# Kernel optimization log

Measured on AMD Instinct MI355X. Metric: run time of the kernel, lower is better.

## Reference

```python
import jax, jax.numpy as jnp
import numpy as np

D_HEAD = 64
KV_HEADS = 8
Q_HEADS = 32
ROPE_BASE = 10000.0


def rope(x):
    # x: (B, S, H, D); pairs are interleaved along last dim, matching torch view(...,D//2,2)
    B, S, H, D = x.shape
    inv_freq = 1.0 / (ROPE_BASE ** (jnp.arange(0, D, 2, dtype=jnp.float32) / D))
    theta = jnp.arange(S, dtype=jnp.float32)[:, None] * inv_freq[None, :]  # (S, D/2)
    cos = jnp.cos(theta)[None, :, None, :]
    sin = jnp.sin(theta)[None, :, None, :]
    xf = x.astype(jnp.float32).reshape(B, S, H, D // 2, 2)
    x1, x2 = xf[..., 0], xf[..., 1]
    out = jnp.stack((x1 * cos - x2 * sin, x1 * sin + x2 * cos), axis=-1)
    return out.reshape(B, S, H, D).astype(x.dtype)


def setup_inputs() -> dict:
    key = jax.random.key(0)
    ks = jax.random.split(key, 5)
    B, S, D = 2, 2048, 2048
    scale = 1.0 / np.sqrt(D)
    return {
        "x": jax.random.normal(ks[0], (B, S, D), dtype=jnp.float32),
        "Wq": jax.random.normal(ks[1], (Q_HEADS * D_HEAD, D), dtype=jnp.float32) * scale,
        "Wk": jax.random.normal(ks[2], (KV_HEADS * D_HEAD, D), dtype=jnp.float32) * scale,
        "Wv": jax.random.normal(ks[3], (KV_HEADS * D_HEAD, D), dtype=jnp.float32) * scale,
        "Wo": jax.random.normal(ks[4], (D, D), dtype=jnp.float32) * scale,
    }


def reference(x, Wq, Wk, Wv, Wo):
    B, S, D = x.shape
    G = Q_HEADS // KV_HEADS  # query heads per kv head

    Q = (x @ Wq.T).reshape(B, S, Q_HEADS, D_HEAD)
    K = (x @ Wk.T).reshape(B, S, KV_HEADS, D_HEAD)
    V = (x @ Wv.T).reshape(B, S, KV_HEADS, D_HEAD)

    Q = rope(Q)
    K = rope(K)

    # (B, KV, G, S, Dh): group g of kv head h corresponds to q head h*G+g,
    # exactly matching repeat_interleave of K/V along head dim.
    Q = Q.transpose(0, 2, 1, 3).reshape(B, KV_HEADS, G, S, D_HEAD)
    K = K.transpose(0, 2, 1, 3)  # (B, KV, S, Dh)
    V = V.transpose(0, 2, 1, 3)

    scores = jnp.einsum("bkgsd,bktd->bkgst", Q, K) / np.sqrt(D_HEAD).astype(np.float32)
    causal_mask = jnp.tril(jnp.ones((S, S), dtype=bool))
    scores = jnp.where(causal_mask, scores, -jnp.inf)
    probs = jax.nn.softmax(scores, axis=-1)
    attn = jnp.einsum("bkgst,bktd->bkgsd", probs, V)

    attn = attn.reshape(B, Q_HEADS, S, D_HEAD).transpose(0, 2, 1, 3).reshape(B, S, D)
    return attn @ Wo.T
```

## Files before the change

### kernel.cpp

```cpp
#include <hip/hip_runtime.h>
#include <stdint.h>

#define S_LEN   2048
#define D_MODEL 2048
#define DKV     512

typedef __attribute__((ext_vector_type(8))) short short8;
typedef __attribute__((ext_vector_type(4))) float f32x4;

__device__ static inline unsigned short f2bf(float f) {
  unsigned u = __builtin_bit_cast(unsigned, f);
  u += 0x7FFFu + ((u >> 16) & 1u);
  return (unsigned short)(u >> 16);
}
__device__ static inline float bf2f(unsigned short h) {
  return __builtin_bit_cast(float, ((unsigned)h) << 16);
}
__device__ static inline unsigned packtrunc2(float f0, float f1) {
  return __builtin_amdgcn_perm(__builtin_bit_cast(unsigned, f1),
                               __builtin_bit_cast(unsigned, f0), 0x07060302u);
}

__device__ static inline void gload_lds16(const void* g, void* lds) {
  __builtin_amdgcn_global_load_lds((const __attribute__((address_space(1))) void*)g,
                                   (__attribute__((address_space(3))) void*)lds,
                                   16, 0, 0);
}

__global__ __launch_bounds__(256) void cvt_all_kernel(
    const float* __restrict__ x, const float* __restrict__ wq, const float* __restrict__ wk,
    const float* __restrict__ wv, const float* __restrict__ wo,
    unsigned short* __restrict__ xb, unsigned short* __restrict__ wqb,
    unsigned short* __restrict__ wkb, unsigned short* __restrict__ wvb,
    unsigned short* __restrict__ wob) {
  int i = blockIdx.x * 256 + threadIdx.x;
  const float* s; unsigned short* d;
  if (i < 1048576)      { s = x;  d = xb;  }
  else if (i < 1572864) { s = wq; d = wqb; i -= 1048576; }
  else if (i < 1703936) { s = wk; d = wkb; i -= 1572864; }
  else if (i < 1835008) { s = wv; d = wvb; i -= 1703936; }
  else                  { s = wo; d = wob; i -= 1835008; }
  const float4 a = ((const float4*)s)[i * 2];
  const float4 b = ((const float4*)s)[i * 2 + 1];
  unsigned short u[8] = {f2bf(a.x), f2bf(a.y), f2bf(a.z), f2bf(a.w),
                         f2bf(b.x), f2bf(b.y), f2bf(b.z), f2bf(b.w)};
  *(uint4*)(d + (size_t)i * 8) = *(const uint4*)u;
}

__device__ static inline void storeC(unsigned short* C, size_t idx, float v) { C[idx] = f2bf(v); }
__device__ static inline void storeC(float* C, size_t idx, float v) { C[idx] = v; }

template <int CMODE, typename CT>
__device__ __forceinline__ void gemm128_body(const unsigned short* A, int lda,
                                             const unsigned short* B, int ldb,
                                             CT* C, int ldc,
                                             int m0, int n0, int Kdim,
                                             unsigned short* As, unsigned short* Bs) {
  const int tid  = threadIdx.x;
  const int lane = tid & 63;
  const int w    = tid >> 6;
  const int wm   = w >> 1, wn = w & 1;
  const int lcol = lane & 15;
  const int lq   = lane >> 4;

  f32x4 acc[4][4] = {};

  for (int k0 = 0; k0 < Kdim; k0 += 32) {
    __syncthreads();
#pragma unroll
    for (int i = 0; i < 2; ++i) {
      const int c  = i * 4 + w;
      const int e  = c * 512 + lane * 8;
      const int rr = e >> 5;
      const int cc = e & 31;
      gload_lds16(A + (size_t)(m0 + rr) * lda + (k0 + cc), As + c * 512);
      gload_lds16(B + (size_t)(n0 + rr) * ldb + (k0 + cc), Bs + c * 512);
    }
    __syncthreads();

    short8 af[4], bfr[4];
#pragma unroll
    for (int mi = 0; mi < 4; ++mi)
      af[mi] = *(const short8*)&As[(wm * 64 + mi * 16 + lcol) * 32 + lq * 8];
#pragma unroll
    for (int ni = 0; ni < 4; ++ni)
      bfr[ni] = *(const short8*)&Bs[(wn * 64 + ni * 16 + lcol) * 32 + lq * 8];
#pragma unroll
    for (int mi = 0; mi < 4; ++mi)
#pragma unroll
      for (int ni = 0; ni < 4; ++ni)
        acc[mi][ni] = __builtin_amdgcn_mfma_f32_16x16x32_bf16(af[mi], bfr[ni], acc[mi][ni], 0, 0, 0);
  }
#pragma unroll
  for (int mi = 0; mi < 4; ++mi)
#pragma unroll
    for (int ni = 0; ni < 4; ++ni)
#pragma unroll
      for (int r = 0; r < 4; ++r) {
        const int row = m0 + wm * 64 + mi * 16 + lq * 4 + r;
        const int col = n0 + wn * 64 + ni * 16 + lcol;
        if constexpr (CMODE == 1) {
          C[((size_t)((row >> 11) * 512 + col)) * 2048 + (row & 2047)] = f2bf(acc[mi][ni][r]);
        } else {
          storeC(C, (size_t)row * ldc + col, acc[mi][ni][r]);
        }
      }
}

__global__ __launch_bounds__(256) void qkv_gemm_kernel(
    const unsigned short* __restrict__ x,
    const unsigned short* __restrict__ Wq, const unsigned short* __restrict__ Wk,
    const unsigned short* __restrict__ Wv,
    unsigned short* __restrict__ Qo, unsigned short* __restrict__ Ko, unsigned short* __restrict__ Vt) {
  __shared__ unsigned short As[128 * 32];
  __shared__ unsigned short Bs[128 * 32];
  const int tn = blockIdx.x;
  const int m0 = blockIdx.y * 128;
  if (tn < 16) {
    gemm128_body<0>(x, D_MODEL, Wq, D_MODEL, Qo, D_MODEL, m0, tn * 128, D_MODEL, As, Bs);
  } else if (tn < 20) {
    gemm128_body<0>(x, D_MODEL, Wk, D_MODEL, Ko, DKV, m0, (tn - 16) * 128, D_MODEL, As, Bs);
  } else {
    gemm128_body<1>(x, D_MODEL, Wv, D_MODEL, Vt, DKV, m0, (tn - 20) * 128, D_MODEL, As, Bs);
  }
}

__global__ __launch_bounds__(256) void oproj_gemm_kernel(
    const unsigned short* __restrict__ A, const unsigned short* __restrict__ Wo,
    float* __restrict__ C) {
  __shared__ unsigned short As[128 * 32];
  __shared__ unsigned short Bs[128 * 32];
  gemm128_body<0>(A, D_MODEL, Wo, D_MODEL, C, D_MODEL,
                  blockIdx.y * 128, blockIdx.x * 128, D_MODEL, As, Bs);
}

__global__ __launch_bounds__(256) void rope_both_kernel(unsigned short* __restrict__ Qb,
                                                        unsigned short* __restrict__ Kb) {
  int idx = blockIdx.x * 256 + threadIdx.x;
  unsigned short* X; int lgHalf; float scale;
  if (idx < 4194304) { X = Qb; lgHalf = 10; scale = 0.1803368801111244f; }
  else               { X = Kb; lgHalf = 8;  scale = 1.0f; idx -= 4194304; }
  const int half = 1 << lgHalf;
  const int r  = idx >> lgHalf;
  const int cp = idx & (half - 1);
  const int i  = cp & 31;
  const int s  = r & (S_LEN - 1);
  const float inv = exp2f(-13.287712379549449f * (float)(2 * i) * (1.0f / 64.0f));
  const float th  = (float)s * inv;
  const float c = cosf(th), sn = sinf(th);
  unsigned short* p = X + ((size_t)r << (lgHalf + 1)) + 2 * cp;
  const float x0 = bf2f(p[0]), x1 = bf2f(p[1]);
  p[0] = f2bf((x0 * c - x1 * sn) * scale);
  p[1] = f2bf((x0 * sn + x1 * c) * scale);
}

__global__ __launch_bounds__(256, 2) void attn_kernel(const unsigned short* __restrict__ Q,
                                                      const unsigned short* __restrict__ K,
                                                      const unsigned short* __restrict__ Vt,
                                                      unsigned short* __restrict__ O) {
  const int hq = blockIdx.y;
  const int bb = blockIdx.z;
  const int hk = hq >> 2;
  const int tid  = threadIdx.x;
  const int lane = tid & 63;
  const int w    = tid >> 6;
  const int lcol = lane & 15;
  const int lq   = lane >> 4;
  const int trow = tid >> 2;
  const int tq   = (tid & 3) * 16;

  const int X = blockIdx.x;
  const int qt[4] = {X, 15 - X, 16 + X, 31 - X};

  __shared__ unsigned short Ks[64 * 72];
  __shared__ unsigned short Vts[64 * 72];
  __shared__ unsigned short Ps[4][64 * 72];

  const int prow = w * 16 + lcol;

  uint4 kp0, kp1, vp0, vp1;
  {
    const unsigned short* gk = K + ((size_t)(bb * S_LEN + trow)) * DKV + hk * 64 + tq;
    kp0 = *(const uint4*)gk; kp1 = *(const uint4*)(gk + 8);
    const unsigned short* gv = Vt + ((size_t)(bb * DKV + hk * 64 + trow)) * S_LEN + tq;
    vp0 = *(const uint4*)gv; vp1 = *(const uint4*)(gv + 8);
  }

#pragma unroll
  for (int j = 0; j < 4; ++j) {
    const unsigned short* g = Q + ((size_t)(bb * S_LEN + qt[j] * 64 + trow)) * D_MODEL + hq * 64 + tq;
    *(uint4*)&Ps[j][trow * 72 + tq]     = *(const uint4*)g;
    *(uint4*)&Ps[j][trow * 72 + tq + 8] = *(const uint4*)(g + 8);
  }
  asm volatile("s_waitcnt lgkmcnt(0)" ::: "memory");

  short8 qf[4][2];
#pragma unroll
  for (int j = 0; j < 4; ++j)
#pragma unroll
    for (int ks = 0; ks < 2; ++ks)
      qf[j][ks] = *(const short8*)&Ps[j][prow * 72 + ks * 32 + lq * 8];

  f32x4 Oacc[4][4] = {};
  float lacc[4] = {0.f, 0.f, 0.f, 0.f};

  const int tmax = qt[3];
  for (int t = 0; t <= tmax; ++t) {
    __syncthreads();
    *(uint4*)&Ks[trow * 72 + tq]      = kp0;
    *(uint4*)&Ks[trow * 72 + tq + 8]  = kp1;
    *(uint4*)&Vts[trow * 72 + tq]     = vp0;
    *(uint4*)&Vts[trow * 72 + tq + 8] = vp1;
    if (t < tmax) {
      const int t1 = (t + 1) * 64;
      const unsigned short* gk = K + ((size_t)(bb * S_LEN + t1 + trow)) * DKV + hk * 64 + tq;
      kp0 = *(const uint4*)gk; kp1 = *(const uint4*)(gk + 8);
      const unsigned short* gv = Vt + ((size_t)(bb * DKV + hk * 64 + trow)) * S_LEN + t1 + tq;
      vp0 = *(const uint4*)gv; vp1 = *(const uint4*)(gv + 8);
    }
    __syncthreads();

    bool act[4];
#pragma unroll
    for (int j = 0; j < 4; ++j) act[j] = (t <= qt[j]);

    f32x4 S[4][4] = {};
#pragma unroll
    for (int ks = 0; ks < 2; ++ks)
#pragma unroll
      for (int nt = 0; nt < 4; ++nt) {
        const short8 kf = *(const short8*)&Ks[(nt * 16 + lcol) * 72 + ks * 32 + lq * 8];
#pragma unroll
        for (int j = 0; j < 4; ++j)
          if (act[j])
            S[j][nt] = __builtin_amdgcn_mfma_f32_16x16x32_bf16(kf, qf[j][ks], S[j][nt], 0, 0, 0);
      }

#pragma unroll
    for (int j = 0; j < 4; ++j) {
      if (!act[j]) continue;
      if (t == qt[j]) {
        const int qrow = qt[j] * 64 + prow;
#pragma unroll
        for (int nt = 0; nt < 4; ++nt)
#pragma unroll
          for (int r = 0; r < 4; ++r) {
            const int key = t * 64 + nt * 16 + lq * 4 + r;
            if (key > qrow) S[j][nt][r] = -1e30f;
          }
      }
#pragma unroll
      for (int nt = 0; nt < 4; ++nt) {
        const float p0 = __builtin_amdgcn_exp2f(S[j][nt][0]);
        const float p1 = __builtin_amdgcn_exp2f(S[j][nt][1]);
        const float p2 = __builtin_amdgcn_exp2f(S[j][nt][2]);
        const float p3 = __builtin_amdgcn_exp2f(S[j][nt][3]);
        lacc[j] += (p0 + p1) + (p2 + p3);
        unsigned u2[2] = {packtrunc2(p0, p1), packtrunc2(p2, p3)};
        *(uint2*)&Ps[j][prow * 72 + nt * 16 + lq * 4] = *(const uint2*)u2;
      }
    }
    asm volatile("s_waitcnt lgkmcnt(0)" ::: "memory");

#pragma unroll
    for (int ks = 0; ks < 2; ++ks) {
      short8 pf[4];
#pragma unroll
      for (int j = 0; j < 4; ++j)
        if (act[j]) pf[j] = *(const short8*)&Ps[j][prow * 72 + ks * 32 + lq * 8];
#pragma unroll
      for (int dt = 0; dt < 4; ++dt) {
        const short8 vf = *(const short8*)&Vts[(dt * 16 + lcol) * 72 + ks * 32 + lq * 8];
#pragma unroll
        for (int j = 0; j < 4; ++j)
          if (act[j])
            Oacc[j][dt] = __builtin_amdgcn_mfma_f32_16x16x32_bf16(vf, pf[j], Oacc[j][dt], 0, 0, 0);
      }
    }
  }

#pragma unroll
  for (int j = 0; j < 4; ++j) {
    float l = lacc[j];
    l += __shfl_xor(l, 16);
    l += __shfl_xor(l, 32);
    const float inv = 1.0f / l;
    const int qrow = qt[j] * 64 + prow;
#pragma unroll
    for (int dt = 0; dt < 4; ++dt) {
      unsigned short u[4] = {f2bf(Oacc[j][dt][0] * inv), f2bf(Oacc[j][dt][1] * inv),
                             f2bf(Oacc[j][dt][2] * inv), f2bf(Oacc[j][dt][3] * inv)};
      *(uint2*)&O[(size_t)(bb * S_LEN + qrow) * D_MODEL + hq * 64 + dt * 16 + lq * 4] =
          *(const uint2*)u;
    }
  }
}

extern "C" void kernel_launch(void* const* d_in, const int* in_sizes, int n_in,
                              void* d_out, int out_size, void* d_ws, size_t ws_size,
                              hipStream_t stream) {
  const float* x  = (const float*)d_in[0];
  const float* Wq = (const float*)d_in[1];
  const float* Wk = (const float*)d_in[2];
  const float* Wv = (const float*)d_in[3];
  const float* Wo = (const float*)d_in[4];
  float* out = (float*)d_out;

  unsigned short* Qb  = (unsigned short*)d_ws;
  unsigned short* Kb  = Qb  + (size_t)4096 * 2048;
  unsigned short* Vtg = Kb  + (size_t)4096 * 512;
  unsigned short* Ab  = Vtg + (size_t)1024 * 2048;
  unsigned short* xb  = Ab  + (size_t)4096 * 2048;
  unsigned short* Wqb = xb  + (size_t)4096 * 2048;
  unsigned short* Wkb = Wqb + (size_t)2048 * 2048;
  unsigned short* Wvb = Wkb + (size_t)512 * 2048;
  unsigned short* Wob = Wvb + (size_t)512 * 2048;

  cvt_all_kernel<<<9216, 256, 0, stream>>>(x, Wq, Wk, Wv, Wo, xb, Wqb, Wkb, Wvb, Wob);

  qkv_gemm_kernel<<<dim3(24, 32), 256, 0, stream>>>(xb, Wqb, Wkb, Wvb, Qb, Kb, Vtg);
  rope_both_kernel<<<20480, 256, 0, stream>>>(Qb, Kb);
  attn_kernel<<<dim3(8, 32, 2), 256, 0, stream>>>(Qb, Kb, Vtg, Ab);
  oproj_gemm_kernel<<<dim3(16, 32), 256, 0, stream>>>(Ab, Wob, out);
}
```

Before: 307.9 us.

## Rewrite QKV and output-projection GEMMs with larger tiles and a 4-stage LDS pipeline

Replaces the 128x128 single-buffered GEMM with 256x256 (QKV) and 128x256 (output projection) tiles run by 512-thread blocks. Global-to-LDS loads are issued three tiles ahead into a 4-buffer ring, paced by explicit vmcnt waits and raw barriers, and the LDS layout is XOR-swizzled to avoid bank conflicts. Block IDs are remapped for L2 locality and MFMA sections are wrapped in raised wave priority. This is meant to hide memory latency and raise data reuse, at the cost of a large dynamic LDS footprint (128KB/96KB), hardcoded K=2048 loop counts and fewer blocks in the grid.

```diff
diff --git a/kernel.cpp b/kernel.cpp
--- a/kernel.cpp
+++ b/kernel.cpp
@@ -25,6 +25,15 @@
   __builtin_amdgcn_global_load_lds((const __attribute__((address_space(1))) void*)g,
                                    (__attribute__((address_space(3))) void*)lds,
                                    16, 0, 0);
+}
+
+template <int N>
+__device__ __forceinline__ void wait_vm() {
+  if constexpr (N == 8)      asm volatile("s_waitcnt vmcnt(8)" ::: "memory");
+  else if constexpr (N == 6) asm volatile("s_waitcnt vmcnt(6)" ::: "memory");
+  else if constexpr (N == 4) asm volatile("s_waitcnt vmcnt(4)" ::: "memory");
+  else if constexpr (N == 3) asm volatile("s_waitcnt vmcnt(3)" ::: "memory");
+  else                       asm volatile("s_waitcnt vmcnt(0)" ::: "memory");
 }
 
 __global__ __launch_bounds__(256) void cvt_all_kernel(
@@ -47,91 +56,146 @@
   *(uint4*)(d + (size_t)i * 8) = *(const uint4*)u;
 }
 
-__device__ static inline void storeC(unsigned short* C, size_t idx, float v) { C[idx] = f2bf(v); }
-__device__ static inline void storeC(float* C, size_t idx, float v) { C[idx] = v; }
-
-template <int CMODE, typename CT>
-__device__ __forceinline__ void gemm128_body(const unsigned short* A, int lda,
-                                             const unsigned short* B, int ldb,
-                                             CT* C, int ldc,
-                                             int m0, int n0, int Kdim,
-                                             unsigned short* As, unsigned short* Bs) {
+template <int BM, int CMODE, typename CT>
+__device__ __forceinline__ void gemm_deep_body(
+    const unsigned short* __restrict__ A, int lda,
+    const unsigned short* __restrict__ B, int ldb,
+    CT* __restrict__ C, int ldc, int m0, int n0, unsigned short* ldsu) {
+  constexpr int MI = BM / 32;
+  constexpr int NI = 4;
+  constexpr int A_BYTES = BM * 64;
+  constexpr int B_BYTES = 256 * 64;
+  constexpr int TILE_BYTES = A_BYTES + B_BYTES;
+  constexpr int AL = BM / 128;
+  constexpr int LOADS = AL + 2;
+  constexpr int VMS = 2 * LOADS;
+
   const int tid  = threadIdx.x;
   const int lane = tid & 63;
   const int w    = tid >> 6;
-  const int wm   = w >> 1, wn = w & 1;
+  const int wm   = w >> 2;
+  const int wn   = w & 3;
   const int lcol = lane & 15;
   const int lq   = lane >> 4;
-
-  f32x4 acc[4][4] = {};
-
-  for (int k0 = 0; k0 < Kdim; k0 += 32) {
-    __syncthreads();
-#pragma unroll
-    for (int i = 0; i < 2; ++i) {
-      const int c  = i * 4 + w;
-      const int e  = c * 512 + lane * 8;
-      const int rr = e >> 5;
-      const int cc = e & 31;
-      gload_lds16(A + (size_t)(m0 + rr) * lda + (k0 + cc), As + c * 512);
-      gload_lds16(B + (size_t)(n0 + rr) * ldb + (k0 + cc), Bs + c * 512);
-    }
-    __syncthreads();
-
-    short8 af[4], bfr[4];
-#pragma unroll
-    for (int mi = 0; mi < 4; ++mi)
-      af[mi] = *(const short8*)&As[(wm * 64 + mi * 16 + lcol) * 32 + lq * 8];
-#pragma unroll
-    for (int ni = 0; ni < 4; ++ni)
-      bfr[ni] = *(const short8*)&Bs[(wn * 64 + ni * 16 + lcol) * 32 + lq * 8];
-#pragma unroll
-    for (int mi = 0; mi < 4; ++mi)
-#pragma unroll
-      for (int ni = 0; ni < 4; ++ni)
+  char* const ldsb = (char*)ldsu;
+
+  const int sl   = (lane & 7) ^ (lane >> 3);
+  const int colg = (sl & 3) * 8;
+  const unsigned short* gA[AL];
+  const unsigned short* gB[2];
+#pragma unroll
+  for (int L = 0; L < AL; ++L) {
+    const int r = 2 * (L * 64 + w * 8 + (lane >> 3)) + (sl >> 2);
+    gA[L] = A + (size_t)(m0 + r) * lda + colg;
+  }
+#pragma unroll
+  for (int L = 0; L < 2; ++L) {
+    const int r = 2 * (L * 64 + w * 8 + (lane >> 3)) + (sl >> 2);
+    gB[L] = B + (size_t)(n0 + r) * ldb + colg;
+  }
+
+  auto stage = [&](int tt) {
+    char* const sb = ldsb + (tt & 3) * TILE_BYTES;
+#pragma unroll
+    for (int L = 0; L < AL; ++L)
+      gload_lds16(gA[L] + tt * 32, sb + L * 8192 + w * 1024);
+#pragma unroll
+    for (int L = 0; L < 2; ++L)
+      gload_lds16(gB[L] + tt * 32, sb + A_BYTES + L * 8192 + w * 1024);
+  };
+
+  const int sR    = (((lcol & 1) << 2) | lq) ^ ((lcol >> 1) & 7);
+  const int rdoff = (lcol >> 1) * 128 + sR * 16;
+
+  f32x4 acc[MI][NI] = {};
+
+  auto compute_tile = [&](char* buf) {
+    short8 af[MI], bfr[NI];
+#pragma unroll
+    for (int mi = 0; mi < MI; ++mi)
+      af[mi] = *(const short8*)(buf + wm * (MI * 1024) + mi * 1024 + rdoff);
+#pragma unroll
+    for (int ni = 0; ni < NI; ++ni)
+      bfr[ni] = *(const short8*)(buf + A_BYTES + wn * 4096 + ni * 1024 + rdoff);
+    __builtin_amdgcn_s_setprio(1);
+#pragma unroll
+    for (int mi = 0; mi < MI; ++mi)
+#pragma unroll
+      for (int ni = 0; ni < NI; ++ni)
         acc[mi][ni] = __builtin_amdgcn_mfma_f32_16x16x32_bf16(af[mi], bfr[ni], acc[mi][ni], 0, 0, 0);
-  }
-#pragma unroll
-  for (int mi = 0; mi < 4; ++mi)
-#pragma unroll
-    for (int ni = 0; ni < 4; ++ni)
+    __builtin_amdgcn_s_setprio(0);
+  };
+
+  stage(0); stage(1); stage(2);
+
+#define GPHASE(T, VMW, DOSTG)                          \
+  do {                                                 \
+    wait_vm<VMW>();                                    \
+    __builtin_amdgcn_s_barrier();                      \
+    asm volatile("" ::: "memory");                     \
+    __builtin_amdgcn_sched_barrier(0);                 \
+    if (DOSTG) stage((T) + 3);                         \
+    compute_tile(ldsb + ((T) & 3) * TILE_BYTES);       \
+  } while (0)
+
+  for (int t4 = 0; t4 < 15; ++t4) {
+    const int t = t4 * 4;
+    GPHASE(t + 0, VMS, true);
+    GPHASE(t + 1, VMS, true);
+    GPHASE(t + 2, VMS, true);
+    GPHASE(t + 3, VMS, true);
+  }
+  GPHASE(60, VMS,   true);
+  GPHASE(61, VMS,   false);
+  GPHASE(62, LOADS, false);
+  GPHASE(63, 0,     false);
+#undef GPHASE
+
+#pragma unroll
+  for (int mi = 0; mi < MI; ++mi)
+#pragma unroll
+    for (int ni = 0; ni < NI; ++ni)
 #pragma unroll
       for (int r = 0; r < 4; ++r) {
-        const int row = m0 + wm * 64 + mi * 16 + lq * 4 + r;
+        const int row = m0 + wm * (MI * 16) + mi * 16 + lq * 4 + r;
         const int col = n0 + wn * 64 + ni * 16 + lcol;
         if constexpr (CMODE == 1) {
           C[((size_t)((row >> 11) * 512 + col)) * 2048 + (row & 2047)] = f2bf(acc[mi][ni][r]);
+        } else if constexpr (CMODE == 2) {
+          C[(size_t)row * ldc + col] = acc[mi][ni][r];
         } else {
-          storeC(C, (size_t)row * ldc + col, acc[mi][ni][r]);
+          C[(size_t)row * ldc + col] = f2bf(acc[mi][ni][r]);
         }
       }
 }
 
-__global__ __launch_bounds__(256) void qkv_gemm_kernel(
+__global__ __launch_bounds__(512, 2) void qkv_gemm_kernel(
     const unsigned short* __restrict__ x,
     const unsigned short* __restrict__ Wq, const unsigned short* __restrict__ Wk,
     const unsigned short* __restrict__ Wv,
-    unsigned short* __restrict__ Qo, unsigned short* __restrict__ Ko, unsigned short* __restrict__ Vt) {
-  __shared__ unsigned short As[128 * 32];
-  __shared__ unsigned short Bs[128 * 32];
-  const int tn = blockIdx.x;
-  const int m0 = blockIdx.y * 128;
-  if (tn < 16) {
-    gemm128_body<0>(x, D_MODEL, Wq, D_MODEL, Qo, D_MODEL, m0, tn * 128, D_MODEL, As, Bs);
-  } else if (tn < 20) {
-    gemm128_body<0>(x, D_MODEL, Wk, D_MODEL, Ko, DKV, m0, (tn - 16) * 128, D_MODEL, As, Bs);
-  } else {
-    gemm128_body<1>(x, D_MODEL, Wv, D_MODEL, Vt, DKV, m0, (tn - 20) * 128, D_MODEL, As, Bs);
-  }
-}
-
-__global__ __launch_bounds__(256) void oproj_gemm_kernel(
+    unsigned short* __restrict__ Qo, unsigned short* __restrict__ Ko,
+    unsigned short* __restrict__ Vt) {
+  extern __shared__ __align__(16) unsigned short lds[];
+  const int bid = blockIdx.x;
+  const int swz = (bid & 7) * 24 + (bid >> 3);
+  const int mt = swz / 12, nt = swz % 12;
+  const int m0 = mt * 256;
+  if (nt < 8)
+    gemm_deep_body<256, 0, unsigned short>(x, D_MODEL, Wq, D_MODEL, Qo, D_MODEL, m0, nt * 256, lds);
+  else if (nt < 10)
+    gemm_deep_body<256, 0, unsigned short>(x, D_MODEL, Wk, D_MODEL, Ko, DKV, m0, (nt - 8) * 256, lds);
+  else
+    gemm_deep_body<256, 1, unsigned short>(x, D_MODEL, Wv, D_MODEL, Vt, DKV, m0, (nt - 10) * 256, lds);
+}
+
+__global__ __launch_bounds__(512, 2) void oproj_gemm_kernel(
     const unsigned short* __restrict__ A, const unsigned short* __restrict__ Wo,
     float* __restrict__ C) {
-  __shared__ unsigned short As[128 * 32];
-  __shared__ unsigned short Bs[128 * 32];
-  gemm128_body<0>(A, D_MODEL, Wo, D_MODEL, C, D_MODEL,
-                  blockIdx.y * 128, blockIdx.x * 128, D_MODEL, As, Bs);
+  extern __shared__ __align__(16) unsigned short lds[];
+  const int bid = blockIdx.x;
+  const int swz = (bid & 7) * 32 + (bid >> 3);
+  const int mt = swz >> 3, nt = swz & 7;
+  gemm_deep_body<128, 2, float>(A, D_MODEL, Wo, D_MODEL, C, D_MODEL, mt * 128, nt * 256, lds);
 }
 
 __global__ __launch_bounds__(256) void rope_both_kernel(unsigned short* __restrict__ Qb,
@@ -316,10 +380,19 @@
   unsigned short* Wvb = Wkb + (size_t)512 * 2048;
   unsigned short* Wob = Wvb + (size_t)512 * 2048;
 
+  static bool attr_set = false;
+  if (!attr_set) {
+    hipFuncSetAttribute(reinterpret_cast<const void*>(qkv_gemm_kernel),
+                        hipFuncAttributeMaxDynamicSharedMemorySize, 131072);
+    hipFuncSetAttribute(reinterpret_cast<const void*>(oproj_gemm_kernel),
+                        hipFuncAttributeMaxDynamicSharedMemorySize, 98304);
+    attr_set = true;
+  }
+
   cvt_all_kernel<<<9216, 256, 0, stream>>>(x, Wq, Wk, Wv, Wo, xb, Wqb, Wkb, Wvb, Wob);
 
-  qkv_gemm_kernel<<<dim3(24, 32), 256, 0, stream>>>(xb, Wqb, Wkb, Wvb, Qb, Kb, Vtg);
+  qkv_gemm_kernel<<<192, 512, 131072, stream>>>(xb, Wqb, Wkb, Wvb, Qb, Kb, Vtg);
   rope_both_kernel<<<20480, 256, 0, stream>>>(Qb, Kb);
   attn_kernel<<<dim3(8, 32, 2), 256, 0, stream>>>(Qb, Kb, Vtg, Ab);
-  oproj_gemm_kernel<<<dim3(16, 32), 256, 0, stream>>>(Ab, Wob, out);
-}
+  oproj_gemm_kernel<<<256, 512, 98304, stream>>>(Ab, Wob, out);
+}
```

After: 286.1 us. 1.08x faster.
